# Kernel optimization log

Measured on AMD Instinct MI355X. Metric: run time of the kernel, lower is better.

The kernel has to match this reference:

```python
import jax, jax.numpy as jnp
import numpy as np

BS, MA, H, NH = 64, 64, 64, 4  # molecules, max atoms per molecule, hsize, n_heads


def _lengths():
    # deterministic ragged molecule sizes in [24, 64]
    return np.array([24 + (7 * i) % 41 for i in range(BS)], dtype=np.int64)


def _scopes():
    lengths = _lengths()
    N = int(lengths.sum())  # 2774
    scope = np.zeros((BS, MA), dtype=np.int64)      # pad slots gather row 0 (zeros)
    rev = np.zeros((N,), dtype=np.int64)            # flat atom -> b*MA + slot
    pos = 1                                          # flat row 0 is the zero pad row
    for b, L in enumerate(lengths):
        scope[b, :L] = np.arange(pos, pos + L)
        rev[pos - 1:pos - 1 + L] = b * MA + np.arange(L)
        pos += L
    return scope, rev, N


def setup_inputs() -> dict:
    key = jax.random.key(0)
    k0, k1, k2, k3 = jax.random.split(key, 4)
    scope, rev, N = _scopes()
    inputs = jax.random.normal(k0, (N + 1, H), dtype=jnp.float32)
    inputs = inputs.at[0].set(0.0)  # zero pad row, as in graphretro flat tensors
    Wa_pair = jax.random.normal(k1, (H, H * NH), dtype=jnp.float32) * (1.0 / np.sqrt(H))
    Wa_score = jax.random.normal(k2, (H, NH), dtype=jnp.float32) * (1.0 / np.sqrt(H))
    W_proj = jax.random.normal(k3, (H * NH, H), dtype=jnp.float32) * (1.0 / np.sqrt(H * NH))
    return {
        "inputs": inputs,
        "scope_tensor": jnp.asarray(scope),
        "scope_rev_tensor": jnp.asarray(rev),
        "Wa_pair": Wa_pair,
        "Wa_score": Wa_score,
        "W_proj": W_proj,
    }


def reference(inputs, scope_tensor, scope_rev_tensor, Wa_pair, Wa_score, W_proj):
    bs, ma = scope_tensor.shape
    h = inputs.shape[1]
    nh = Wa_score.shape[1]
    # flat_to_batch: [bs, ma, h]; pad slots pull the zero row 0
    c_batch = inputs[scope_tensor]
    # get_pair: pairwise sum of atom embeddings -> [bs, ma, ma, h]
    atom_pair = c_batch[:, :, None, :] + c_batch[:, None, :, :]
    # Wa_pair (no bias) + relu, viewed as [bs, ma, ma, h, nh]
    total_att = jax.nn.relu(atom_pair @ Wa_pair).reshape(bs, ma, ma, h, nh)
    # einsum '...hn,hjn->...jn' with j==1, then sigmoid -> [bs, ma, ma, nh]
    att_score = jax.nn.sigmoid(jnp.einsum('bijhn,hn->bijn', total_att, Wa_score))
    # att_score * c_atom[b,j,h], summed over j -> [bs, ma, h, nh]
    c_sum = jnp.einsum('bijn,bjh->bihn', att_score, c_batch)
    # view to [bs, ma, h*nh] (h-major, matching torch .view) and project
    c_atom_att = c_sum.reshape(bs, ma, h * nh) @ W_proj  # [bs, ma, h]
    c_mol_att = c_atom_att.sum(axis=1)  # [bs, h]
    # batch_to_flat + prepend zero row -> [N+1, h]
    flat = c_atom_att.reshape(bs * ma, h)[scope_rev_tensor]
    c_atom_att_flat = jnp.concatenate([jnp.zeros((1, h), flat.dtype), flat], axis=0)
    return (c_mol_att, c_atom_att_flat)
```

## Files before the change

### kernel.cpp

```cpp
#include <hip/hip_runtime.h>
#include <stdint.h>

typedef _Float16 h2 __attribute__((ext_vector_type(2)));
typedef _Float16 h8 __attribute__((ext_vector_type(8)));
typedef float f32x4 __attribute__((ext_vector_type(4)));
typedef unsigned int u32;
typedef unsigned short u16;

#define WT_STR 68
#define PJ_STR 68
#define WP_STR 268
#define PI_STR 36
#define CB_STR 72
#define CT_STR 68
#define AB_STR 72
#define CS_STR 264
#define WS_STR 36

__device__ __forceinline__ u32 pk2(float a, float b) {
    return __builtin_bit_cast(u32, __builtin_amdgcn_cvt_pkrtz(a, b));
}
__device__ __forceinline__ h8 frag4(u32 a, u32 b, u32 c, u32 d) {
    return __builtin_bit_cast(h8, make_uint4(a, b, c, d));
}

__global__ __launch_bounds__(512, 1) void atom_attn(
    const float* __restrict__ inputs,
    const int*   __restrict__ scope,
    const float* __restrict__ Wa_pair,
    const float* __restrict__ Wa_score,
    const float* __restrict__ W_proj,
    float* __restrict__ out_mol,
    float* __restrict__ out_flat)
{
    __shared__ __align__(16) u16 s_wa[256 * WT_STR];
    __shared__ __align__(16) u16 s_pj[256 * PJ_STR];
    __shared__ __align__(16) u16 s_wp[64 * WP_STR];
    __shared__ __align__(16) u32 s_pi[4 * 16 * PI_STR];
    __shared__ __align__(16) u16 s_cb[64 * CB_STR];
    __shared__ __align__(16) u16 s_ct[64 * CT_STR];
    __shared__ __align__(16) u16 s_ab[64 * AB_STR];
    __shared__ __align__(16) u16 s_cs[16 * CS_STR];
    __shared__ __align__(16) u32 s_ws[4 * WS_STR];

    const int t = threadIdx.x;
    const int w = t >> 6, l = t & 63;
    const int ml = l & 15, q = l >> 4;
    const int b = blockIdx.y, bx = blockIdx.x;
    const int i_base = bx * 16;

    if (t < 256) {
        if (t < 128) {
            const int n = t & 3, hh = t >> 2;
            const float g0 = Wa_score[(2 * hh) * 4 + n];
            const float g1 = Wa_score[(2 * hh + 1) * 4 + n];
            s_ws[n * WS_STR + hh] = pk2(g0, g1);
        }
        {
            const int jp = (t & 31) * 2;
            const int pp = t >> 5;
            const int r0 = scope[b * 64 + jp];
            const int r1 = scope[b * 64 + jp + 1];
            const f32x4 a0 = *(const f32x4*)(inputs + (size_t)r0 * 64 + pp * 8);
            const f32x4 a1 = *(const f32x4*)(inputs + (size_t)r0 * 64 + pp * 8 + 4);
            const f32x4 b0 = *(const f32x4*)(inputs + (size_t)r1 * 64 + pp * 8);
            const f32x4 b1 = *(const f32x4*)(inputs + (size_t)r1 * 64 + pp * 8 + 4);
            float A[8] = {a0[0], a0[1], a0[2], a0[3], a1[0], a1[1], a1[2], a1[3]};
            float B[8] = {b0[0], b0[1], b0[2], b0[3], b1[0], b1[1], b1[2], b1[3]};
            *(uint4*)&s_cb[jp * CB_STR + pp * 8] =
                make_uint4(pk2(A[0], A[1]), pk2(A[2], A[3]), pk2(A[4], A[5]), pk2(A[6], A[7]));
            *(uint4*)&s_cb[(jp + 1) * CB_STR + pp * 8] =
                make_uint4(pk2(B[0], B[1]), pk2(B[2], B[3]), pk2(B[4], B[5]), pk2(B[6], B[7]));
            #pragma unroll
            for (int e = 0; e < 8; ++e)
                *(u32*)&s_ct[(pp * 8 + e) * CT_STR + jp] = pk2(A[e], B[e]);
        }
        {
            const int o0 = (t & 31) * 2, seg = t >> 5;
            #pragma unroll
            for (int k2 = 0; k2 < 16; ++k2) {
                const int c0 = seg * 32 + k2 * 2;
                const float2 r0 = *(const float2*)(W_proj + c0 * 64 + o0);
                const float2 r1 = *(const float2*)(W_proj + (c0 + 1) * 64 + o0);
                *(u32*)&s_wp[o0 * WP_STR + c0]       = pk2(r0.x, r1.x);
                *(u32*)&s_wp[(o0 + 1) * WP_STR + c0] = pk2(r0.y, r1.y);
            }
        }
    } else {
        const int t2 = t & 255;
        const int cg = (t2 & 127) * 2;
        const int hh2 = t2 >> 7;
        const int cp0 = (cg & 3) * 64 + (cg >> 2);
        #pragma unroll
        for (int k2 = 0; k2 < 16; ++k2) {
            const int h0 = hh2 * 32 + k2 * 2;
            const float2 r0 = *(const float2*)(Wa_pair + h0 * 256 + cg);
            const float2 r1 = *(const float2*)(Wa_pair + (h0 + 1) * 256 + cg);
            *(u32*)&s_wa[cp0 * WT_STR + h0]        = pk2(r0.x, r1.x);
            *(u32*)&s_wa[(cp0 + 64) * WT_STR + h0] = pk2(r0.y, r1.y);
        }
    }
    __syncthreads();

    {
        const int mq = w & 3, jh = w >> 2;
        f32x4 D[4][2];
        #pragma unroll
        for (int k = 0; k < 4; ++k) { D[k][0] = (f32x4)0.f; D[k][1] = (f32x4)0.f; }
        h8 bf[2][2];
        #pragma unroll
        for (int jt = 0; jt < 2; ++jt)
            #pragma unroll
            for (int ks = 0; ks < 2; ++ks)
                bf[jt][ks] = __builtin_bit_cast(h8,
                    *(const uint4*)&s_cb[((jh * 2 + jt) * 16 + ml) * CB_STR + ks * 32 + q * 8]);
        #pragma unroll
        for (int k = 0; k < 4; ++k) {
            const int mt = mq * 4 + k;
            #pragma unroll
            for (int ks = 0; ks < 2; ++ks) {
                const uint2 x0 = *(const uint2*)&s_wa[(mt * 16 + ml) * WT_STR + ks * 32 + q * 8];
                const uint2 x1 = *(const uint2*)&s_wa[(mt * 16 + ml) * WT_STR + ks * 32 + q * 8 + 4];
                const h8 af = frag4(x0.x, x0.y, x1.x, x1.y);
                D[k][0] = __builtin_amdgcn_mfma_f32_16x16x32_f16(af, bf[0][ks], D[k][0], 0, 0, 0);
                D[k][1] = __builtin_amdgcn_mfma_f32_16x16x32_f16(af, bf[1][ks], D[k][1], 0, 0, 0);
            }
        }
        #pragma unroll
        for (int k = 0; k < 4; ++k) {
            const int mt = mq * 4 + k;
            const int nb = mt >> 2, h0 = (mt & 3) * 16 + q * 4;
            #pragma unroll
            for (int jt = 0; jt < 2; ++jt) {
                const int jtile = jh * 2 + jt;
                const int j = jtile * 16 + ml;
                const u32 p0 = pk2(D[k][jt][0], D[k][jt][1]);
                const u32 p1 = pk2(D[k][jt][2], D[k][jt][3]);
                *(uint2*)&s_pj[(nb * 64 + j) * PJ_STR + h0] = make_uint2(p0, p1);
                if (jtile == bx)
                    *(uint2*)&s_pi[(nb * 16 + ml) * PI_STR + (h0 >> 1)] = make_uint2(p0, p1);
            }
        }
    }
    __syncthreads();

    {
        const int n = w & 3, ih = w >> 2;
        u32 pj_u[32];
        #pragma unroll
        for (int k = 0; k < 16; ++k) {
            const uint2 v = *(const uint2*)&s_pj[(n * 64 + l) * PJ_STR + k * 4];
            pj_u[2 * k] = v.x; pj_u[2 * k + 1] = v.y;
        }
        u32 ws_u[32];
        #pragma unroll
        for (int k = 0; k < 8; ++k) {
            const uint4 v = *(const uint4*)&s_ws[n * WS_STR + k * 4];
            ws_u[4 * k] = v.x; ws_u[4 * k + 1] = v.y; ws_u[4 * k + 2] = v.z; ws_u[4 * k + 3] = v.w;
        }
        const h2 zero2 = {(_Float16)0.f, (_Float16)0.f};
        #pragma unroll
        for (int ii = 0; ii < 8; ++ii) {
            const int iloc = ih * 8 + ii;
            const u32* pir = &s_pi[(n * 16 + iloc) * PI_STR];
            float s0 = 0.f, s1 = 0.f;
            #pragma unroll
            for (int c8 = 0; c8 < 8; ++c8) {
                const uint4 pv = *(const uint4*)&pir[c8 * 4];
                const u32 pe[4] = {pv.x, pv.y, pv.z, pv.w};
                #pragma unroll
                for (int e = 0; e < 4; ++e) {
                    const h2 pi2 = __builtin_bit_cast(h2, pe[e]);
                    const h2 pj2 = __builtin_bit_cast(h2, pj_u[c8 * 4 + e]);
                    h2 tv = pi2 + pj2;
                    tv = __builtin_elementwise_max(tv, zero2);
                    if (e & 1)
                        s1 = __builtin_amdgcn_fdot2(tv,
                                __builtin_bit_cast(h2, ws_u[c8 * 4 + e]), s1, false);
                    else
                        s0 = __builtin_amdgcn_fdot2(tv,
                                __builtin_bit_cast(h2, ws_u[c8 * 4 + e]), s0, false);
                }
            }
            const float s = s0 + s1;
            const float a = 1.f / (1.f + __expf(-s));
            const _Float16 ah = (_Float16)a;
            s_ab[(iloc * 4 + n) * AB_STR + l] = __builtin_bit_cast(u16, ah);
        }
    }
    __syncthreads();

    {
        const int mt3 = w & 3, nh = w >> 2;
        h8 af3[2];
        #pragma unroll
        for (int ks = 0; ks < 2; ++ks)
            af3[ks] = __builtin_bit_cast(h8,
                *(const uint4*)&s_ab[(mt3 * 16 + ml) * AB_STR + ks * 32 + q * 8]);
        #pragma unroll
        for (int nx = 0; nx < 2; ++nx) {
            const int nt = nh * 2 + nx;
            f32x4 D2 = (f32x4)0.f;
            #pragma unroll
            for (int ks = 0; ks < 2; ++ks) {
                const uint2 y0 = *(const uint2*)&s_ct[(nt * 16 + ml) * CT_STR + ks * 32 + q * 8];
                const uint2 y1 = *(const uint2*)&s_ct[(nt * 16 + ml) * CT_STR + ks * 32 + q * 8 + 4];
                const h8 bfc = frag4(y0.x, y0.y, y1.x, y1.y);
                D2 = __builtin_amdgcn_mfma_f32_16x16x32_f16(af3[ks], bfc, D2, 0, 0, 0);
            }
            const int iloc = mt3 * 4 + q, h = nt * 16 + ml;
            *(uint2*)&s_cs[iloc * CS_STR + h * 4] =
                make_uint2(pk2(D2[0], D2[1]), pk2(D2[2], D2[3]));
        }
    }
    __syncthreads();

    if (w < 4) {
        f32x4 D4 = (f32x4)0.f;
        #pragma unroll
        for (int ks = 0; ks < 8; ++ks) {
            const h8 af = __builtin_bit_cast(h8,
                *(const uint4*)&s_cs[ml * CS_STR + ks * 32 + q * 8]);
            const uint2 z0 = *(const uint2*)&s_wp[(w * 16 + ml) * WP_STR + ks * 32 + q * 8];
            const uint2 z1 = *(const uint2*)&s_wp[(w * 16 + ml) * WP_STR + ks * 32 + q * 8 + 4];
            const h8 bf4 = frag4(z0.x, z0.y, z1.x, z1.y);
            D4 = __builtin_amdgcn_mfma_f32_16x16x32_f16(af, bf4, D4, 0, 0, 0);
        }
        const int o = w * 16 + ml;
        #pragma unroll
        for (int r = 0; r < 4; ++r) {
            const int iloc = q * 4 + r;
            const int row = scope[b * 64 + i_base + iloc];
            if (row > 0) out_flat[(size_t)row * 64 + o] = D4[r];
        }
        float s4 = D4[0] + D4[1] + D4[2] + D4[3];
        s4 += __shfl_xor(s4, 16, 64);
        s4 += __shfl_xor(s4, 32, 64);
        if (l < 16) atomicAdd(out_mol + b * 64 + o, s4);
    }
}

extern "C" void kernel_launch(void* const* d_in, const int* in_sizes, int n_in,
                              void* d_out, int out_size, void* d_ws, size_t ws_size,
                              hipStream_t stream) {
    const float* inputs   = (const float*)d_in[0];
    const int*   scope    = (const int*)d_in[1];
    const float* Wa_pair  = (const float*)d_in[3];
    const float* Wa_score = (const float*)d_in[4];
    const float* W_proj   = (const float*)d_in[5];
    float* out = (float*)d_out;

    (void)hipMemsetAsync(d_out, 0, (64 * 64 + 64) * sizeof(float), stream);

    dim3 grid(4, 64);
    atom_attn<<<grid, 512, 0, stream>>>(inputs, scope, Wa_pair, Wa_score,
                                        W_proj, out, out + 64 * 64);
}
```

Before: 74.59 us.

## Alias shared buffers to shrink LDS and run more blocks per CU

Measured after the change: 74.83 us. About the same (+0.3%).

```diff
diff --git a/kernel.cpp b/kernel.cpp
--- a/kernel.cpp
+++ b/kernel.cpp
@@ -10,7 +10,6 @@
 #define WT_STR 68
 #define PJ_STR 68
 #define WP_STR 268
-#define PI_STR 36
 #define CB_STR 72
 #define CT_STR 68
 #define AB_STR 72
@@ -24,7 +23,7 @@
     return __builtin_bit_cast(h8, make_uint4(a, b, c, d));
 }
 
-__global__ __launch_bounds__(512, 1) void atom_attn(
+__global__ __launch_bounds__(512, 4) void atom_attn(
     const float* __restrict__ inputs,
     const int*   __restrict__ scope,
     const float* __restrict__ Wa_pair,
@@ -33,13 +32,10 @@
     float* __restrict__ out_mol,
     float* __restrict__ out_flat)
 {
-    __shared__ __align__(16) u16 s_wa[256 * WT_STR];
-    __shared__ __align__(16) u16 s_pj[256 * PJ_STR];
-    __shared__ __align__(16) u16 s_wp[64 * WP_STR];
-    __shared__ __align__(16) u32 s_pi[4 * 16 * PI_STR];
+    __shared__ __align__(16) u16 s_big[256 * WT_STR];
     __shared__ __align__(16) u16 s_cb[64 * CB_STR];
     __shared__ __align__(16) u16 s_ct[64 * CT_STR];
-    __shared__ __align__(16) u16 s_ab[64 * AB_STR];
+    __shared__ __align__(16) u16 s_ab[32 * AB_STR];
     __shared__ __align__(16) u16 s_cs[16 * CS_STR];
     __shared__ __align__(16) u32 s_ws[4 * WS_STR];
 
@@ -47,7 +43,7 @@
     const int w = t >> 6, l = t & 63;
     const int ml = l & 15, q = l >> 4;
     const int b = blockIdx.y, bx = blockIdx.x;
-    const int i_base = bx * 16;
+    const int i_base = bx * 8;
 
     if (t < 256) {
         if (t < 128) {
@@ -56,36 +52,23 @@
             const float g1 = Wa_score[(2 * hh + 1) * 4 + n];
             s_ws[n * WS_STR + hh] = pk2(g0, g1);
         }
-        {
-            const int jp = (t & 31) * 2;
-            const int pp = t >> 5;
-            const int r0 = scope[b * 64 + jp];
-            const int r1 = scope[b * 64 + jp + 1];
-            const f32x4 a0 = *(const f32x4*)(inputs + (size_t)r0 * 64 + pp * 8);
-            const f32x4 a1 = *(const f32x4*)(inputs + (size_t)r0 * 64 + pp * 8 + 4);
-            const f32x4 b0 = *(const f32x4*)(inputs + (size_t)r1 * 64 + pp * 8);
-            const f32x4 b1 = *(const f32x4*)(inputs + (size_t)r1 * 64 + pp * 8 + 4);
-            float A[8] = {a0[0], a0[1], a0[2], a0[3], a1[0], a1[1], a1[2], a1[3]};
-            float B[8] = {b0[0], b0[1], b0[2], b0[3], b1[0], b1[1], b1[2], b1[3]};
-            *(uint4*)&s_cb[jp * CB_STR + pp * 8] =
-                make_uint4(pk2(A[0], A[1]), pk2(A[2], A[3]), pk2(A[4], A[5]), pk2(A[6], A[7]));
-            *(uint4*)&s_cb[(jp + 1) * CB_STR + pp * 8] =
-                make_uint4(pk2(B[0], B[1]), pk2(B[2], B[3]), pk2(B[4], B[5]), pk2(B[6], B[7]));
-            #pragma unroll
-            for (int e = 0; e < 8; ++e)
-                *(u32*)&s_ct[(pp * 8 + e) * CT_STR + jp] = pk2(A[e], B[e]);
-        }
-        {
-            const int o0 = (t & 31) * 2, seg = t >> 5;
-            #pragma unroll
-            for (int k2 = 0; k2 < 16; ++k2) {
-                const int c0 = seg * 32 + k2 * 2;
-                const float2 r0 = *(const float2*)(W_proj + c0 * 64 + o0);
-                const float2 r1 = *(const float2*)(W_proj + (c0 + 1) * 64 + o0);
-                *(u32*)&s_wp[o0 * WP_STR + c0]       = pk2(r0.x, r1.x);
-                *(u32*)&s_wp[(o0 + 1) * WP_STR + c0] = pk2(r0.y, r1.y);
-            }
-        }
+        const int jp = (t & 31) * 2;
+        const int pp = t >> 5;
+        const int r0 = scope[b * 64 + jp];
+        const int r1 = scope[b * 64 + jp + 1];
+        const f32x4 a0 = *(const f32x4*)(inputs + (size_t)r0 * 64 + pp * 8);
+        const f32x4 a1 = *(const f32x4*)(inputs + (size_t)r0 * 64 + pp * 8 + 4);
+        const f32x4 b0 = *(const f32x4*)(inputs + (size_t)r1 * 64 + pp * 8);
+        const f32x4 b1 = *(const f32x4*)(inputs + (size_t)r1 * 64 + pp * 8 + 4);
+        float A[8] = {a0[0], a0[1], a0[2], a0[3], a1[0], a1[1], a1[2], a1[3]};
+        float B[8] = {b0[0], b0[1], b0[2], b0[3], b1[0], b1[1], b1[2], b1[3]};
+        *(uint4*)&s_cb[jp * CB_STR + pp * 8] =
+            make_uint4(pk2(A[0], A[1]), pk2(A[2], A[3]), pk2(A[4], A[5]), pk2(A[6], A[7]));
+        *(uint4*)&s_cb[(jp + 1) * CB_STR + pp * 8] =
+            make_uint4(pk2(B[0], B[1]), pk2(B[2], B[3]), pk2(B[4], B[5]), pk2(B[6], B[7]));
+        #pragma unroll
+        for (int e = 0; e < 8; ++e)
+            *(u32*)&s_ct[(pp * 8 + e) * CT_STR + jp] = pk2(A[e], B[e]);
     } else {
         const int t2 = t & 255;
         const int cg = (t2 & 127) * 2;
@@ -96,17 +79,24 @@
             const int h0 = hh2 * 32 + k2 * 2;
             const float2 r0 = *(const float2*)(Wa_pair + h0 * 256 + cg);
             const float2 r1 = *(const float2*)(Wa_pair + (h0 + 1) * 256 + cg);
-            *(u32*)&s_wa[cp0 * WT_STR + h0]        = pk2(r0.x, r1.x);
-            *(u32*)&s_wa[(cp0 + 64) * WT_STR + h0] = pk2(r0.y, r1.y);
+            *(u32*)&s_big[cp0 * WT_STR + h0]        = pk2(r0.x, r1.x);
+            *(u32*)&s_big[(cp0 + 64) * WT_STR + h0] = pk2(r0.y, r1.y);
         }
     }
     __syncthreads();
 
     {
         const int mq = w & 3, jh = w >> 2;
-        f32x4 D[4][2];
-        #pragma unroll
-        for (int k = 0; k < 4; ++k) { D[k][0] = (f32x4)0.f; D[k][1] = (f32x4)0.f; }
+        uint2 afx[4][2][2];
+        #pragma unroll
+        for (int k = 0; k < 4; ++k) {
+            const int mt = mq * 4 + k;
+            #pragma unroll
+            for (int ks = 0; ks < 2; ++ks) {
+                afx[k][ks][0] = *(const uint2*)&s_big[(mt * 16 + ml) * WT_STR + ks * 32 + q * 8];
+                afx[k][ks][1] = *(const uint2*)&s_big[(mt * 16 + ml) * WT_STR + ks * 32 + q * 8 + 4];
+            }
+        }
         h8 bf[2][2];
         #pragma unroll
         for (int jt = 0; jt < 2; ++jt)
@@ -114,31 +104,29 @@
             for (int ks = 0; ks < 2; ++ks)
                 bf[jt][ks] = __builtin_bit_cast(h8,
                     *(const uint4*)&s_cb[((jh * 2 + jt) * 16 + ml) * CB_STR + ks * 32 + q * 8]);
+        __syncthreads();
+
+        f32x4 D[4][2];
+        #pragma unroll
+        for (int k = 0; k < 4; ++k) { D[k][0] = (f32x4)0.f; D[k][1] = (f32x4)0.f; }
+        #pragma unroll
+        for (int k = 0; k < 4; ++k)
+            #pragma unroll
+            for (int ks = 0; ks < 2; ++ks) {
+                const h8 af = frag4(afx[k][ks][0].x, afx[k][ks][0].y,
+                                    afx[k][ks][1].x, afx[k][ks][1].y);
+                D[k][0] = __builtin_amdgcn_mfma_f32_16x16x32_f16(af, bf[0][ks], D[k][0], 0, 0, 0);
+                D[k][1] = __builtin_amdgcn_mfma_f32_16x16x32_f16(af, bf[1][ks], D[k][1], 0, 0, 0);
+            }
         #pragma unroll
         for (int k = 0; k < 4; ++k) {
             const int mt = mq * 4 + k;
-            #pragma unroll
-            for (int ks = 0; ks < 2; ++ks) {
-                const uint2 x0 = *(const uint2*)&s_wa[(mt * 16 + ml) * WT_STR + ks * 32 + q * 8];
-                const uint2 x1 = *(const uint2*)&s_wa[(mt * 16 + ml) * WT_STR + ks * 32 + q * 8 + 4];
-                const h8 af = frag4(x0.x, x0.y, x1.x, x1.y);
-                D[k][0] = __builtin_amdgcn_mfma_f32_16x16x32_f16(af, bf[0][ks], D[k][0], 0, 0, 0);
-                D[k][1] = __builtin_amdgcn_mfma_f32_16x16x32_f16(af, bf[1][ks], D[k][1], 0, 0, 0);
-            }
-        }
-        #pragma unroll
-        for (int k = 0; k < 4; ++k) {
-            const int mt = mq * 4 + k;
-            const int nb = mt >> 2, h0 = (mt & 3) * 16 + q * 4;
+            const int h0 = (mt & 3) * 16 + q * 4;
             #pragma unroll
             for (int jt = 0; jt < 2; ++jt) {
-                const int jtile = jh * 2 + jt;
-                const int j = jtile * 16 + ml;
-                const u32 p0 = pk2(D[k][jt][0], D[k][jt][1]);
-                const u32 p1 = pk2(D[k][jt][2], D[k][jt][3]);
-                *(uint2*)&s_pj[(nb * 64 + j) * PJ_STR + h0] = make_uint2(p0, p1);
-                if (jtile == bx)
-                    *(uint2*)&s_pi[(nb * 16 + ml) * PI_STR + (h0 >> 1)] = make_uint2(p0, p1);
+                const int j = (jh * 2 + jt) * 16 + ml;
+                *(uint2*)&s_big[(mq * 64 + j) * PJ_STR + h0] =
+                    make_uint2(pk2(D[k][jt][0], D[k][jt][1]), pk2(D[k][jt][2], D[k][jt][3]));
             }
         }
     }
@@ -149,7 +137,7 @@
         u32 pj_u[32];
         #pragma unroll
         for (int k = 0; k < 16; ++k) {
-            const uint2 v = *(const uint2*)&s_pj[(n * 64 + l) * PJ_STR + k * 4];
+            const uint2 v = *(const uint2*)&s_big[(n * 64 + l) * PJ_STR + k * 4];
             pj_u[2 * k] = v.x; pj_u[2 * k + 1] = v.y;
         }
         u32 ws_u[32];
@@ -160,14 +148,15 @@
         }
         const h2 zero2 = {(_Float16)0.f, (_Float16)0.f};
         #pragma unroll
-        for (int ii = 0; ii < 8; ++ii) {
-            const int iloc = ih * 8 + ii;
-            const u32* pir = &s_pi[(n * 16 + iloc) * PI_STR];
+        for (int ii = 0; ii < 4; ++ii) {
+            const int iloc = ih * 4 + ii;
+            const u16* pir = &s_big[(n * 64 + i_base + iloc) * PJ_STR];
             float s0 = 0.f, s1 = 0.f;
             #pragma unroll
             for (int c8 = 0; c8 < 8; ++c8) {
-                const uint4 pv = *(const uint4*)&pir[c8 * 4];
-                const u32 pe[4] = {pv.x, pv.y, pv.z, pv.w};
+                const uint2 v0 = *(const uint2*)&pir[c8 * 8];
+                const uint2 v1 = *(const uint2*)&pir[c8 * 8 + 4];
+                const u32 pe[4] = {v0.x, v0.y, v1.x, v1.y};
                 #pragma unroll
                 for (int e = 0; e < 4; ++e) {
                     const h2 pi2 = __builtin_bit_cast(h2, pe[e]);
@@ -191,27 +180,31 @@
     __syncthreads();
 
     {
-        const int mt3 = w & 3, nh = w >> 2;
-        h8 af3[2];
-        #pragma unroll
-        for (int ks = 0; ks < 2; ++ks)
-            af3[ks] = __builtin_bit_cast(h8,
+        const int o0 = (t & 31) * 2, seg = t >> 5;
+        #pragma unroll
+        for (int k2 = 0; k2 < 8; ++k2) {
+            const int c0 = seg * 16 + k2 * 2;
+            const float2 r0 = *(const float2*)(W_proj + c0 * 64 + o0);
+            const float2 r1 = *(const float2*)(W_proj + (c0 + 1) * 64 + o0);
+            *(u32*)&s_big[o0 * WP_STR + c0]       = pk2(r0.x, r1.x);
+            *(u32*)&s_big[(o0 + 1) * WP_STR + c0] = pk2(r0.y, r1.y);
+        }
+    }
+    {
+        const int mt3 = w & 1, nt = w >> 1;
+        f32x4 D2 = (f32x4)0.f;
+        #pragma unroll
+        for (int ks = 0; ks < 2; ++ks) {
+            const h8 af = __builtin_bit_cast(h8,
                 *(const uint4*)&s_ab[(mt3 * 16 + ml) * AB_STR + ks * 32 + q * 8]);
-        #pragma unroll
-        for (int nx = 0; nx < 2; ++nx) {
-            const int nt = nh * 2 + nx;
-            f32x4 D2 = (f32x4)0.f;
-            #pragma unroll
-            for (int ks = 0; ks < 2; ++ks) {
-                const uint2 y0 = *(const uint2*)&s_ct[(nt * 16 + ml) * CT_STR + ks * 32 + q * 8];
-                const uint2 y1 = *(const uint2*)&s_ct[(nt * 16 + ml) * CT_STR + ks * 32 + q * 8 + 4];
-                const h8 bfc = frag4(y0.x, y0.y, y1.x, y1.y);
-                D2 = __builtin_amdgcn_mfma_f32_16x16x32_f16(af3[ks], bfc, D2, 0, 0, 0);
-            }
-            const int iloc = mt3 * 4 + q, h = nt * 16 + ml;
-            *(uint2*)&s_cs[iloc * CS_STR + h * 4] =
-                make_uint2(pk2(D2[0], D2[1]), pk2(D2[2], D2[3]));
-        }
+            const uint2 y0 = *(const uint2*)&s_ct[(nt * 16 + ml) * CT_STR + ks * 32 + q * 8];
+            const uint2 y1 = *(const uint2*)&s_ct[(nt * 16 + ml) * CT_STR + ks * 32 + q * 8 + 4];
+            const h8 bfc = frag4(y0.x, y0.y, y1.x, y1.y);
+            D2 = __builtin_amdgcn_mfma_f32_16x16x32_f16(af, bfc, D2, 0, 0, 0);
+        }
+        const int iloc = mt3 * 4 + q, h = nt * 16 + ml;
+        *(uint2*)&s_cs[iloc * CS_STR + h * 4] =
+            make_uint2(pk2(D2[0], D2[1]), pk2(D2[2], D2[3]));
     }
     __syncthreads();
 
@@ -221,19 +214,21 @@
         for (int ks = 0; ks < 8; ++ks) {
             const h8 af = __builtin_bit_cast(h8,
                 *(const uint4*)&s_cs[ml * CS_STR + ks * 32 + q * 8]);
-            const uint2 z0 = *(const uint2*)&s_wp[(w * 16 + ml) * WP_STR + ks * 32 + q * 8];
-            const uint2 z1 = *(const uint2*)&s_wp[(w * 16 + ml) * WP_STR + ks * 32 + q * 8 + 4];
+            const uint2 z0 = *(const uint2*)&s_big[(w * 16 + ml) * WP_STR + ks * 32 + q * 8];
+            const uint2 z1 = *(const uint2*)&s_big[(w * 16 + ml) * WP_STR + ks * 32 + q * 8 + 4];
             const h8 bf4 = frag4(z0.x, z0.y, z1.x, z1.y);
             D4 = __builtin_amdgcn_mfma_f32_16x16x32_f16(af, bf4, D4, 0, 0, 0);
         }
         const int o = w * 16 + ml;
-        #pragma unroll
-        for (int r = 0; r < 4; ++r) {
-            const int iloc = q * 4 + r;
-            const int row = scope[b * 64 + i_base + iloc];
-            if (row > 0) out_flat[(size_t)row * 64 + o] = D4[r];
-        }
-        float s4 = D4[0] + D4[1] + D4[2] + D4[3];
+        if (q < 2) {
+            #pragma unroll
+            for (int r = 0; r < 4; ++r) {
+                const int iloc = q * 4 + r;
+                const int row = scope[b * 64 + i_base + iloc];
+                if (row > 0) out_flat[(size_t)row * 64 + o] = D4[r];
+            }
+        }
+        float s4 = (q < 2) ? (D4[0] + D4[1] + D4[2] + D4[3]) : 0.f;
         s4 += __shfl_xor(s4, 16, 64);
         s4 += __shfl_xor(s4, 32, 64);
         if (l < 16) atomicAdd(out_mol + b * 64 + o, s4);
@@ -252,7 +247,7 @@
 
     (void)hipMemsetAsync(d_out, 0, (64 * 64 + 64) * sizeof(float), stream);
 
-    dim3 grid(4, 64);
+    dim3 grid(8, 64);
     atom_attn<<<grid, 512, 0, stream>>>(inputs, scope, Wa_pair, Wa_score,
                                         W_proj, out, out + 64 * 64);
 }
```
